# Kernel tuning notes

Measured on AMD Instinct MI355X. Metric: run time of the kernel, lower is better.

Reference implementation:

```python
import jax, jax.numpy as jnp
import numpy as np

D_MODEL = 2048
N_HEADS = 16
D_HEAD = 128
D_LATENT = 512


def setup_inputs() -> dict:
    key = jax.random.key(0)
    ks = jax.random.split(key, 5)
    s = lambda fan_in: 1.0 / np.sqrt(fan_in)
    x = jax.random.normal(ks[0], (2, 2048, D_MODEL), dtype=jnp.float32)
    # nn.Linear weights stored as [out, in]; we keep [in, out] for x @ W
    W_q = jax.random.uniform(ks[1], (D_MODEL, N_HEADS * D_HEAD), jnp.float32, -s(D_MODEL), s(D_MODEL))
    W_kv_down = jax.random.uniform(ks[2], (D_MODEL, D_LATENT), jnp.float32, -s(D_MODEL), s(D_MODEL))
    W_kv_up = jax.random.uniform(ks[3], (D_LATENT, N_HEADS * D_HEAD), jnp.float32, -s(D_LATENT), s(D_LATENT))
    W_o = jax.random.uniform(ks[4], (N_HEADS * D_HEAD, D_MODEL), jnp.float32, -s(N_HEADS * D_HEAD), s(N_HEADS * D_HEAD))
    return {"x": x, "W_q": W_q, "W_kv_down": W_kv_down, "W_kv_up": W_kv_up, "W_o": W_o}


def reference(x, W_q, W_kv_down, W_kv_up, W_o):
    B, S, _ = x.shape
    # q: [B, H, S, Dh]
    q = (x @ W_q).reshape(B, S, N_HEADS, D_HEAD).transpose(0, 2, 1, 3)
    # latent compression then up-projection; shared K = V
    latent = x @ W_kv_down                      # [B, S, Dl]
    kv = (latent @ W_kv_up).reshape(B, S, N_HEADS, D_HEAD).transpose(0, 2, 1, 3)
    scale = 1.0 / np.sqrt(D_HEAD).astype(np.float32)
    scores = jnp.einsum('bhqd,bhkd->bhqk', q, kv) * scale  # [B,H,S,S]
    probs = jax.nn.softmax(scores, axis=-1)
    out = jnp.einsum('bhqk,bhkd->bhqd', probs, kv)          # [B,H,S,Dh]
    out = out.transpose(0, 2, 1, 3).reshape(B, S, N_HEADS * D_HEAD)
    return out @ W_o
```

## Files before the change

### kernel.cpp

```cpp
#include <hip/hip_runtime.h>

typedef __attribute__((ext_vector_type(8))) __bf16 bf16x8;
typedef __attribute__((ext_vector_type(4))) float f32x4;
typedef __attribute__((ext_vector_type(8))) unsigned short u16x8;
typedef __attribute__((ext_vector_type(4))) unsigned short u16x4;
typedef __attribute__((ext_vector_type(2))) unsigned int u32x2;
typedef __attribute__((ext_vector_type(4))) unsigned int u32x4;

#define MFMA16(a, b, c) __builtin_amdgcn_mfma_f32_16x16x32_bf16((a), (b), (c), 0, 0, 0)

__device__ __forceinline__ unsigned short f2bf(float f) {
    unsigned int u = __float_as_uint(f);
    unsigned int r = (u + 0x7FFFu + ((u >> 16) & 1u)) >> 16;
    return (unsigned short)r;
}

__device__ __forceinline__ float fexp2(float x) {
#if __has_builtin(__builtin_amdgcn_exp2f)
    return __builtin_amdgcn_exp2f(x);
#else
    return exp2f(x);
#endif
}

__device__ __forceinline__ u32x2 plswap32(unsigned int x, unsigned int y) {
#if __has_builtin(__builtin_amdgcn_permlane32_swap)
    return __builtin_amdgcn_permlane32_swap(x, y, false, false);
#else
    asm volatile("s_nop 1\n\tv_permlane32_swap_b32 %0, %1" : "+v"(x), "+v"(y));
    u32x2 r = {x, y};
    return r;
#endif
}
__device__ __forceinline__ u32x2 plswap16(unsigned int x, unsigned int y) {
#if __has_builtin(__builtin_amdgcn_permlane16_swap)
    return __builtin_amdgcn_permlane16_swap(x, y, false, false);
#else
    asm volatile("s_nop 1\n\tv_permlane16_swap_b32 %0, %1" : "+v"(x), "+v"(y));
    u32x2 r = {x, y};
    return r;
#endif
}

__device__ __forceinline__ float quad_reduce(float v) {
    u32x2 a = plswap32(__float_as_uint(v), __float_as_uint(v));
    v = __uint_as_float(a.x) + __uint_as_float(a.y);
    u32x2 b = plswap16(__float_as_uint(v), __float_as_uint(v));
    return __uint_as_float(b.x) + __uint_as_float(b.y);
}

__device__ __forceinline__ void transpose_tile(const float* __restrict__ in,
                                               unsigned short* __restrict__ out,
                                               int R, int C, int bx, int by) {
    __shared__ float tile[32][33];
    const int tx = threadIdx.x & 31, ty = threadIdx.x >> 5;
    const int c0 = bx * 32, r0 = by * 32;
#pragma unroll
    for (int i = 0; i < 4; ++i)
        tile[ty + i * 8][tx] = in[(size_t)(r0 + ty + i * 8) * C + c0 + tx];
    __syncthreads();
#pragma unroll
    for (int i = 0; i < 4; ++i)
        out[(size_t)(c0 + ty + i * 8) * R + r0 + tx] = f2bf(tile[tx][ty + i * 8]);
}

__global__ __launch_bounds__(256) void k_prep(const float* __restrict__ x,
                                              const float* __restrict__ Wq,
                                              const float* __restrict__ Wkvd,
                                              const float* __restrict__ Wkvu,
                                              const float* __restrict__ Wo,
                                              unsigned short* __restrict__ xb,
                                              unsigned short* __restrict__ Wcat_t,
                                              unsigned short* __restrict__ Wkvu_t,
                                              unsigned short* __restrict__ Wo_t) {
    const int i = blockIdx.x;
    if (i < 8192) {
        const int idx = i * 256 + threadIdx.x;
        const float4 v = ((const float4*)x)[idx];
        u16x4 o = { f2bf(v.x), f2bf(v.y), f2bf(v.z), f2bf(v.w) };
        ((u16x4*)xb)[idx] = o;
    } else if (i < 12288) {
        const int j = i - 8192;
        transpose_tile(Wq, Wcat_t, 2048, 2048, j & 63, j >> 6);
    } else if (i < 13312) {
        const int j = i - 12288;
        transpose_tile(Wkvd, Wcat_t + 2048 * 2048, 2048, 512, j & 15, j >> 4);
    } else if (i < 14336) {
        const int j = i - 13312;
        transpose_tile(Wkvu, Wkvu_t, 512, 2048, j & 63, j >> 6);
    } else {
        const int j = i - 14336;
        transpose_tile(Wo, Wo_t, 2048, 2048, j & 63, j >> 6);
    }
}

template <int OUT_MODE>
__global__ __launch_bounds__(256) void k_gemm_bt(const unsigned short* __restrict__ A,
                                                 const unsigned short* __restrict__ B,
                                                 void* __restrict__ Cv,
                                                 unsigned short* __restrict__ Ct,
                                                 int M, int N, int K, float alpha) {
    __shared__ alignas(16) unsigned short As[2 * 128 * 32];
    __shared__ alignas(16) unsigned short Bs[2 * 128 * 32];
    const int tid = threadIdx.x;
    const int wave = tid >> 6;
    const int lane = tid & 63;
    const int l16 = lane & 15;
    const int quad = lane >> 4;
    const int bm = blockIdx.x * 128;
    const int bn = blockIdx.y * 128;
    const int wm = (wave >> 1) * 64;
    const int wn = (wave & 1) * 64;

    const f32x4 fzero = {0.f, 0.f, 0.f, 0.f};
    f32x4 acc[4][4];
#pragma unroll
    for (int i = 0; i < 4; ++i)
#pragma unroll
        for (int j = 0; j < 4; ++j) acc[i][j] = fzero;

    auto AsL = (__attribute__((address_space(3))) unsigned short*)As;
    auto BsL = (__attribute__((address_space(3))) unsigned short*)Bs;

    const int c0 = wave * 128 + lane;

    auto stage = [&](int kt32) {
        const int boff = (kt32 & 1) * (128 * 32);
        const int kt = kt32 * 32;
#pragma unroll
        for (int j = 0; j < 2; ++j) {
            const int c = c0 + j * 64;
            __builtin_amdgcn_global_load_lds(
                (const __attribute__((address_space(1))) void*)(A + (size_t)(bm + (c >> 2)) * K + kt + (c & 3) * 8),
                (__attribute__((address_space(3))) void*)(AsL + boff + c * 8), 16, 0, 0);
            __builtin_amdgcn_global_load_lds(
                (const __attribute__((address_space(1))) void*)(B + (size_t)(bn + (c >> 2)) * K + kt + (c & 3) * 8),
                (__attribute__((address_space(3))) void*)(BsL + boff + c * 8), 16, 0, 0);
        }
    };

    const int nk = K >> 5;
    stage(0);
    for (int kt32 = 0; kt32 < nk; ++kt32) {
        __syncthreads();
        if (kt32 + 1 < nk) stage(kt32 + 1);
        const unsigned short* Ab = As + (kt32 & 1) * (128 * 32);
        const unsigned short* Bb = Bs + (kt32 & 1) * (128 * 32);

        bf16x8 af[4], bfr[4];
#pragma unroll
        for (int mt = 0; mt < 4; ++mt)
            af[mt] = *(const bf16x8*)(Ab + (wm + mt * 16 + l16) * 32 + quad * 8);
#pragma unroll
        for (int nt = 0; nt < 4; ++nt)
            bfr[nt] = *(const bf16x8*)(Bb + (wn + nt * 16 + l16) * 32 + quad * 8);
#pragma unroll
        for (int mt = 0; mt < 4; ++mt)
#pragma unroll
            for (int nt = 0; nt < 4; ++nt)
                acc[mt][nt] = MFMA16(af[mt], bfr[nt], acc[mt][nt]);
    }

#pragma unroll
    for (int mt = 0; mt < 4; ++mt)
#pragma unroll
        for (int nt = 0; nt < 4; ++nt) {
            const int row0 = bm + wm + mt * 16 + quad * 4;
            const int col = bn + wn + nt * 16 + l16;
            u16x4 pk;
#pragma unroll
            for (int r = 0; r < 4; ++r) {
                const float v0 = acc[mt][nt][r];
                if (OUT_MODE == 0) {
                    ((float*)Cv)[(size_t)(row0 + r) * N + col] = v0 * alpha;
                } else if (OUT_MODE == 3) {
                    if (col < 2048)
                        ((unsigned short*)Cv)[(size_t)(row0 + r) * 2048 + col] = f2bf(v0 * alpha);
                    else
                        Ct[(size_t)(row0 + r) * 512 + (col - 2048)] = f2bf(v0);
                } else {
                    const unsigned short b = f2bf(v0 * alpha);
                    ((unsigned short*)Cv)[(size_t)(row0 + r) * N + col] = b;
                    pk[r] = b;
                }
            }
            if (OUT_MODE == 2) {
                const size_t ti =
                    ((size_t)((row0 >> 11) * (N >> 7) + (col >> 7)) * 128 + (col & 127)) * 2048 +
                    (row0 & 2047);
                *(u16x4*)(Ct + ti) = pk;
            }
        }
}

__global__ __launch_bounds__(256, 2) void k_attn(const unsigned short* __restrict__ Q,
                                                 const unsigned short* __restrict__ KV,
                                                 const unsigned short* __restrict__ KVT,
                                                 unsigned short* __restrict__ O) {
    __shared__ alignas(16) unsigned short Ks[2 * 64 * 128];
    __shared__ alignas(16) unsigned short Vt[2 * 128 * 64];

    const int tid = threadIdx.x;
    const int wave = tid >> 6, lane = tid & 63;
    const int l16 = lane & 15, quad = lane >> 4;
    const int l8 = l16 & 7;
    const int lid = blockIdx.x + (blockIdx.y << 4);
    const int wid = ((lid & 7) << 6) + (lid >> 3);
    const int qt = wid & 15;
    const int bh = wid >> 4;
    const size_t tokbase = (size_t)(bh >> 4) * 2048;
    const int hcol = (bh & 15) * 128;
    const unsigned short* kvt_head = KVT + (size_t)bh * (128 * 2048);

    bf16x8 qf[2][4];
    const int qrow0 = qt * 128 + wave * 32;
#pragma unroll
    for (int nt = 0; nt < 2; ++nt) {
        const unsigned short* qp =
            Q + (tokbase + qrow0 + nt * 16 + l16) * 2048 + hcol + quad * 8;
#pragma unroll
        for (int kd = 0; kd < 4; ++kd) qf[nt][kd] = *(const bf16x8*)(qp + kd * 32);
    }

    const f32x4 fzero = {0.f, 0.f, 0.f, 0.f};
    f32x4 o_acc[8][2];
#pragma unroll
    for (int dt = 0; dt < 8; ++dt)
#pragma unroll
        for (int nt = 0; nt < 2; ++nt) o_acc[dt][nt] = fzero;
    float l_i[2] = {0.f, 0.f};

    const int krow = tid >> 4, kchunk = tid & 15;
    const int vrow = tid >> 3, vchunk = tid & 7;

    const unsigned short* kvp = KV + (tokbase + krow) * 2048 + hcol + kchunk * 8;
    const unsigned short* vtp = kvt_head + (size_t)vrow * 2048 + vchunk * 8;

    u16x8 kR[4], vR[4];
    auto load_tile = [&]() {
#pragma unroll
        for (int p = 0; p < 4; ++p) {
            kR[p] = *(const u16x8*)(kvp + p * (16 * 2048));
            vR[p] = *(const u16x8*)(vtp + p * (32 * 2048));
        }
        kvp += 64 * 2048;
        vtp += 64;
    };
    auto store_tile = [&](int kt) {
        unsigned short* Kb = Ks + (kt & 1) * (64 * 128);
        unsigned short* Vb = Vt + (kt & 1) * (128 * 64);
#pragma unroll
        for (int p = 0; p < 4; ++p) {
            const int r = p * 16 + krow;
            const int swk = (kchunk & 8) | ((kchunk & 7) ^ (r & 7));
            *(u16x8*)(Kb + r * 128 + swk * 8) = kR[p];
            const int d = p * 32 + vrow;
            const int swv = vchunk ^ (d & 7);
            *(u16x8*)(Vb + d * 64 + swv * 8) = vR[p];
        }
    };

    load_tile();
    store_tile(0);
    load_tile();

    for (int kt = 0; kt < 32; ++kt) {
        __syncthreads();
        if (kt < 31) {
            store_tile(kt + 1);
            if (kt < 30) load_tile();
        }
        const unsigned short* Kb = Ks + (kt & 1) * (64 * 128);
        const unsigned short* Vb = Vt + (kt & 1) * (128 * 64);

        f32x4 st[4][2];
#pragma unroll
        for (int mt = 0; mt < 4; ++mt)
#pragma unroll
            for (int nt = 0; nt < 2; ++nt) st[mt][nt] = fzero;
        __builtin_amdgcn_s_setprio(1);
#pragma unroll
        for (int kd = 0; kd < 4; ++kd)
#pragma unroll
            for (int mt = 0; mt < 4; ++mt) {
                const int c = kd * 4 + quad;
                const int sw = (c & 8) | ((c & 7) ^ l8);
                const bf16x8 kf = *(const bf16x8*)(Kb + (mt * 16 + l16) * 128 + sw * 8);
                st[mt][0] = MFMA16(kf, qf[0][kd], st[mt][0]);
                st[mt][1] = MFMA16(kf, qf[1][kd], st[mt][1]);
            }
        __builtin_amdgcn_s_setprio(0);

        bf16x8 pfr[2][2];
#pragma unroll
        for (int nt = 0; nt < 2; ++nt) {
            float p[4][4];
            float rs = 0.f;
#pragma unroll
            for (int mt = 0; mt < 4; ++mt)
#pragma unroll
                for (int r = 0; r < 4; ++r) {
                    p[mt][r] = fexp2(st[mt][nt][r]);
                    rs += p[mt][r];
                }
            l_i[nt] += rs;
#pragma unroll
            for (int s = 0; s < 2; ++s) {
                unsigned int aw0, aw1, bw0, bw1;
                asm("v_cvt_pk_bf16_f32 %0, %1, %2" : "=v"(aw0) : "v"(p[2 * s][0]), "v"(p[2 * s][1]));
                asm("v_cvt_pk_bf16_f32 %0, %1, %2" : "=v"(aw1) : "v"(p[2 * s][2]), "v"(p[2 * s][3]));
                asm("v_cvt_pk_bf16_f32 %0, %1, %2" : "=v"(bw0) : "v"(p[2 * s + 1][0]), "v"(p[2 * s + 1][1]));
                asm("v_cvt_pk_bf16_f32 %0, %1, %2" : "=v"(bw1) : "v"(p[2 * s + 1][2]), "v"(p[2 * s + 1][3]));
                const u32x2 e0 = plswap32(aw0, bw0);
                const u32x2 e1 = plswap32(aw1, bw1);
                const u32x2 f0 = plswap16(e0.x, e0.y);
                const u32x2 f1 = plswap16(e1.x, e1.y);
                const u32x4 w = {f0.x, f1.x, f0.y, f1.y};
                pfr[s][nt] = __builtin_bit_cast(bf16x8, w);
            }
        }

        __builtin_amdgcn_s_setprio(1);
#pragma unroll
        for (int s = 0; s < 2; ++s) {
            const int sw = ((s * 4 + quad) ^ l8) * 8;
            bf16x8 vf[8];
#pragma unroll
            for (int dt = 0; dt < 8; ++dt)
                vf[dt] = *(const bf16x8*)(Vb + (dt * 16 + l16) * 64 + sw);
#pragma unroll
            for (int dt = 0; dt < 8; ++dt) {
                o_acc[dt][0] = MFMA16(vf[dt], pfr[s][0], o_acc[dt][0]);
                o_acc[dt][1] = MFMA16(vf[dt], pfr[s][1], o_acc[dt][1]);
            }
        }
        __builtin_amdgcn_s_setprio(0);
    }

#pragma unroll
    for (int nt = 0; nt < 2; ++nt) {
        const float inv = 1.0f / quad_reduce(l_i[nt]);
        unsigned short* dst = O + (tokbase + qrow0 + nt * 16 + l16) * 2048 + hcol;
#pragma unroll
        for (int dt = 0; dt < 8; ++dt) {
            u16x4 pk;
#pragma unroll
            for (int r = 0; r < 4; ++r) pk[r] = f2bf(o_acc[dt][nt][r] * inv);
            *(u16x4*)(dst + dt * 16 + quad * 4) = pk;
        }
    }
}

extern "C" void kernel_launch(void* const* d_in, const int* in_sizes, int n_in,
                              void* d_out, int out_size, void* d_ws, size_t ws_size,
                              hipStream_t stream) {
    const float* x = (const float*)d_in[0];
    const float* W_q = (const float*)d_in[1];
    const float* W_kvd = (const float*)d_in[2];
    const float* W_kvu = (const float*)d_in[3];
    const float* W_o = (const float*)d_in[4];

    char* w = (char*)d_ws;
    unsigned short* xb = (unsigned short*)(w);
    unsigned short* kvT = xb;
    unsigned short* qb = (unsigned short*)(w + (size_t)16 * 1024 * 1024);
    unsigned short* kvb = (unsigned short*)(w + (size_t)32 * 1024 * 1024);
    unsigned short* Wo_t = (unsigned short*)(w + (size_t)48 * 1024 * 1024);
    unsigned short* Wcat_t = (unsigned short*)(w + (size_t)56 * 1024 * 1024);
    unsigned short* Wkvu_t = (unsigned short*)(w + (size_t)66 * 1024 * 1024);
    unsigned short* lat = (unsigned short*)(w + (size_t)68 * 1024 * 1024);

    k_prep<<<18432, 256, 0, stream>>>(x, W_q, W_kvd, W_kvu, W_o, xb, Wcat_t, Wkvu_t, Wo_t);

    k_gemm_bt<3><<<dim3(32, 20), 256, 0, stream>>>(xb, Wcat_t, qb, lat, 4096, 2560, 2048,
                                                   0.12751743f);
    k_gemm_bt<2><<<dim3(32, 16), 256, 0, stream>>>(lat, Wkvu_t, kvb, kvT, 4096, 2048, 512,
                                                   1.0f);
    k_attn<<<dim3(16, 32), 256, 0, stream>>>(qb, kvb, kvT, qb);
    k_gemm_bt<0><<<dim3(32, 16), 256, 0, stream>>>(qb, Wo_t, d_out, nullptr, 4096, 2048, 2048,
                                                   1.0f);
}
```

Baseline: 309.6 us.

## Stage K/V tiles with direct global-to-LDS loads instead of register staging

Replaces the register-staged copy of K and transposed-V tiles (global load into registers, then a swizzled LDS store) with `__builtin_amdgcn_global_load_lds` 16-byte transfers that write straight into LDS. The XOR swizzle moves from the LDS store address to the global source address, so each lane writes a contiguous LDS slot. The intent is to cut VGPR pressure and the ds_write instructions in the attention main loop, which could help occupancy and instruction issue. In exchange, prefetch depth drops from two tiles in flight to one. Correctness also depends on the barrier waiting for the outstanding LDS-DMA writes.

```diff
diff --git a/kernel.cpp b/kernel.cpp
--- a/kernel.cpp
+++ b/kernel.cpp
@@ -230,46 +230,37 @@
         for (int nt = 0; nt < 2; ++nt) o_acc[dt][nt] = fzero;
     float l_i[2] = {0.f, 0.f};
 
-    const int krow = tid >> 4, kchunk = tid & 15;
-    const int vrow = tid >> 3, vchunk = tid & 7;
-
-    const unsigned short* kvp = KV + (tokbase + krow) * 2048 + hcol + kchunk * 8;
-    const unsigned short* vtp = kvt_head + (size_t)vrow * 2048 + vchunk * 8;
-
-    u16x8 kR[4], vR[4];
-    auto load_tile = [&]() {
+    auto KsL = (__attribute__((address_space(3))) unsigned short*)Ks;
+    auto VtL = (__attribute__((address_space(3))) unsigned short*)Vt;
+
+    const int r4 = tid >> 4, cdK = tid & 15;
+    const int csK = (cdK & 8) | ((cdK & 7) ^ (r4 & 7));
+    const int dv = tid >> 3, cvV = tid & 7;
+    const int csV = cvV ^ (dv & 7);
+    const unsigned short* kp0 = KV + (tokbase + r4) * 2048 + hcol + csK * 8;
+    const unsigned short* vp0 = kvt_head + (size_t)dv * 2048 + csV * 8;
+
+    auto stage = [&](int kt) {
+        auto Kb = KsL + (kt & 1) * (64 * 128) + tid * 8;
+        auto Vb = VtL + (kt & 1) * (128 * 64) + tid * 8;
+        const unsigned short* kp = kp0 + (size_t)kt * (64 * 2048);
+        const unsigned short* vp = vp0 + kt * 64;
 #pragma unroll
         for (int p = 0; p < 4; ++p) {
-            kR[p] = *(const u16x8*)(kvp + p * (16 * 2048));
-            vR[p] = *(const u16x8*)(vtp + p * (32 * 2048));
-        }
-        kvp += 64 * 2048;
-        vtp += 64;
+            __builtin_amdgcn_global_load_lds(
+                (const __attribute__((address_space(1))) void*)(kp + p * (16 * 2048)),
+                (__attribute__((address_space(3))) void*)(Kb + p * 2048), 16, 0, 0);
+            __builtin_amdgcn_global_load_lds(
+                (const __attribute__((address_space(1))) void*)(vp + (size_t)p * (32 * 2048)),
+                (__attribute__((address_space(3))) void*)(Vb + p * 2048), 16, 0, 0);
+        }
     };
-    auto store_tile = [&](int kt) {
-        unsigned short* Kb = Ks + (kt & 1) * (64 * 128);
-        unsigned short* Vb = Vt + (kt & 1) * (128 * 64);
-#pragma unroll
-        for (int p = 0; p < 4; ++p) {
-            const int r = p * 16 + krow;
-            const int swk = (kchunk & 8) | ((kchunk & 7) ^ (r & 7));
-            *(u16x8*)(Kb + r * 128 + swk * 8) = kR[p];
-            const int d = p * 32 + vrow;
-            const int swv = vchunk ^ (d & 7);
-            *(u16x8*)(Vb + d * 64 + swv * 8) = vR[p];
-        }
-    };
-
-    load_tile();
-    store_tile(0);
-    load_tile();
+
+    stage(0);
 
     for (int kt = 0; kt < 32; ++kt) {
         __syncthreads();
-        if (kt < 31) {
-            store_tile(kt + 1);
-            if (kt < 30) load_tile();
-        }
+        if (kt < 31) stage(kt + 1);
         const unsigned short* Kb = Ks + (kt & 1) * (64 * 128);
         const unsigned short* Vb = Vt + (kt & 1) * (128 * 64);
 
```

Result: no change. 306.4 us (-1.0%).
